# Kernel optimization log

Hardware: AMD Instinct MI355X
Metric: run time of the kernel (lower is better)

Reference implementation:

```python
import jax, jax.numpy as jnp
import numpy as np

HEADS = 4
DIM_HEAD = 128
HIDDEN = HEADS * DIM_HEAD  # 512
DIM = 256
EMBED = 256


def mish(x):
    return x * jnp.tanh(jax.nn.softplus(x))


def setup_inputs() -> dict:
    key = jax.random.key(0)
    k = jax.random.split(key, 7)
    b, a, f, t = 64, 8, DIM, 256
    x = jax.random.normal(k[0], (b, a, f, t), dtype=jnp.float32)
    time = jax.random.normal(k[1], (b, a, EMBED), dtype=jnp.float32)
    # to_qkv: Conv2d(dim, 3*hidden, 1, bias=False) -> weight [3*hidden, dim]
    w_qkv = jax.random.normal(k[2], (3 * HIDDEN, DIM), dtype=jnp.float32) * (1.0 / np.sqrt(DIM))
    # time_mlp: Mish -> Linear(embed, 3*hidden)
    w_time = jax.random.normal(k[3], (3 * HIDDEN, EMBED), dtype=jnp.float32) * (1.0 / np.sqrt(EMBED))
    b_time = jax.random.normal(k[4], (3 * HIDDEN,), dtype=jnp.float32) * 0.01
    # to_out: Conv2d(hidden, dim, 1) with bias
    w_out = jax.random.normal(k[5], (DIM, HIDDEN), dtype=jnp.float32) * (1.0 / np.sqrt(HIDDEN))
    b_out = jax.random.normal(k[6], (DIM,), dtype=jnp.float32) * 0.01
    return {"x": x, "time": time, "w_qkv": w_qkv, "w_time": w_time,
            "b_time": b_time, "w_out": w_out, "b_out": b_out}


def reference(x, time, w_qkv, w_time, b_time, w_out, b_out):
    b, a, f, t = x.shape
    heads, c = HEADS, DIM_HEAD
    # x: b a f t -> b f a t (channels-first for 1x1 conv)
    xp = jnp.transpose(x, (0, 2, 1, 3))  # [b, f, a, t]
    # 1x1 conv == channel GEMM
    qkv = jnp.einsum('of,bfat->boat', w_qkv, xp)  # [b, 3*hidden, a, t]
    # time MLP: Mish -> Linear; bias broadcast over t
    temb = mish(time) @ w_time.T + b_time          # [b, a, 3*hidden]
    temb = jnp.transpose(temb, (0, 2, 1))[..., None]  # [b, 3*hidden, a, 1]
    qkv = qkv + temb
    # 'b (qkv heads c) h w -> qkv (b h) heads c w' with h=a, w=t
    qkv = qkv.reshape(b, 3, heads, c, a, t)
    qkv = jnp.transpose(qkv, (1, 0, 4, 2, 3, 5)).reshape(3, b * a, heads, c, t)
    q, k, v = qkv[0], qkv[1], qkv[2]  # each [(b a), heads, c, t]
    k = jax.nn.softmax(k, axis=-1)
    # linear attention: context over keys/values, then apply to q
    context = jnp.einsum('bhdn,bhen->bhde', k, v)   # [(b a), heads, c, c]
    out = jnp.einsum('bhde,bhdn->bhen', context, q)  # [(b a), heads, c, t]
    # '(b h) heads c w -> b (heads c) h w'
    out = out.reshape(b, a, heads * c, t)
    out = jnp.transpose(out, (0, 2, 1, 3))  # [b, hidden, a, t]
    out = jnp.einsum('of,bfat->boat', w_out, out) + b_out[None, :, None, None]
    # b f a t -> b a f t
    return jnp.transpose(out, (0, 2, 1, 3))
```

## Files before the change

### kernel.cpp

```cpp
#include <hip/hip_runtime.h>

typedef __bf16 bf16;
typedef __bf16 bf16x4 __attribute__((ext_vector_type(4)));
typedef __bf16 bf16x8 __attribute__((ext_vector_type(8)));
typedef float  f32x4  __attribute__((ext_vector_type(4)));

#define TT    256
#define FF    256
#define NS    512

#define TSTR3 36
#define TSZ3  (128 * TSTR3)

#define SCHED0 __builtin_amdgcn_sched_barrier(0)
#define BAR    __builtin_amdgcn_s_barrier()
#define WAITVM(N) asm volatile("s_waitcnt vmcnt(" #N ")" ::: "memory")
#define WAITLGKM0 asm volatile("s_waitcnt lgkmcnt(0)" ::: "memory")
#define SP1 __builtin_amdgcn_s_setprio(1)
#define SP0 __builtin_amdgcn_s_setprio(0)

static __device__ inline f32x4 mfma16(bf16x8 a, bf16x8 b, f32x4 c) {
    return __builtin_amdgcn_mfma_f32_16x16x32_bf16(a, b, c, 0, 0, 0);
}

typedef const __attribute__((address_space(1))) unsigned int* gp_t;
typedef __attribute__((address_space(3))) unsigned int* lp_t;
static __device__ inline void gll16(const bf16* g, bf16* l) {
    __builtin_amdgcn_global_load_lds((gp_t)g, (lp_t)l, 16, 0, 0);
}


static __device__ inline void stage128g(const bf16* __restrict__ g, int ld, bf16* __restrict__ l) {
    int lane = threadIdx.x & 63, wv = threadIdx.x >> 6;
    int r = lane >> 2;
    int c8 = ((lane & 3) ^ ((lane >> 3) & 3)) * 8;
#pragma unroll
    for (int i = 0; i < 2; i++) {
        int row0 = wv * 32 + i * 16;
        gll16(g + (size_t)(row0 + r) * ld + c8, l + row0 * 32);
    }
}
static __device__ inline void stage8(const bf16* __restrict__ g, int ld, bf16* __restrict__ l) {
    int lane = threadIdx.x & 63, wv = threadIdx.x >> 6;
    int r = lane >> 2;
    int c8 = ((lane & 3) ^ ((lane >> 3) & 3)) * 8;
    int row0 = wv * 16;
    gll16(g + (size_t)(row0 + r) * ld + c8, l + row0 * 32);
}
static __device__ inline bf16x8 fragld(const bf16* __restrict__ l, int row0) {
    int lane = threadIdx.x & 63;
    int r15 = lane & 15;
    int kg = (lane >> 4) ^ ((r15 >> 1) & 3);
    return *(const bf16x8*)(l + (row0 + r15) * 32 + kg * 8);
}
static __device__ inline bf16x8 fragld_s(const bf16* __restrict__ l, int row0, int stride) {
    int lane = threadIdx.x & 63;
    return *(const bf16x8*)(l + (row0 + (lane & 15)) * stride + (lane >> 4) * 8);
}

__global__ __launch_bounds__(256) void k_cvt(const float4* __restrict__ src, bf16* __restrict__ dst) {
    int i = blockIdx.x * 256 + threadIdx.x;
    float4 v = src[i];
    bf16x4 o;
    o[0] = (__bf16)v.x; o[1] = (__bf16)v.y; o[2] = (__bf16)v.z; o[3] = (__bf16)v.w;
    *(bf16x4*)(dst + (size_t)i * 4) = o;
}

__global__ __launch_bounds__(256) void k_mish(const float4* __restrict__ src, bf16* __restrict__ dst) {
    int i = blockIdx.x * 256 + threadIdx.x;
    float4 v = src[i];
    float in[4] = {v.x, v.y, v.z, v.w};
    bf16x4 o;
#pragma unroll
    for (int j = 0; j < 4; j++) {
        float sp = log1pf(__expf(in[j]));
        o[j] = (__bf16)(in[j] * tanhf(sp));
    }
    *(bf16x4*)(dst + (size_t)i * 4) = o;
}

__global__ __launch_bounds__(256) void k_xpose(const float* __restrict__ x, bf16* __restrict__ xT) {
    __shared__ float tile[64][65];
    int bid = blockIdx.x;
    int s  = bid >> 4;
    int f0 = ((bid >> 2) & 3) * 64;
    int t0 = (bid & 3) * 64;
    int tid = threadIdx.x;
    int rr = tid >> 4;
    int cc = (tid & 15) * 4;
    const float* xp = x + ((size_t)(s * FF + f0)) * TT + t0;
#pragma unroll
    for (int i = 0; i < 4; i++) {
        int r = i * 16 + rr;
        float4 v = *(const float4*)(xp + (size_t)r * TT + cc);
        tile[r][cc] = v.x; tile[r][cc + 1] = v.y; tile[r][cc + 2] = v.z; tile[r][cc + 3] = v.w;
    }
    __syncthreads();
    bf16* op = xT + ((size_t)(s * TT + t0)) * FF + f0;
#pragma unroll
    for (int i = 0; i < 4; i++) {
        int tr = i * 16 + rr;
        bf16x4 o;
        o[0] = (__bf16)tile[cc][tr];     o[1] = (__bf16)tile[cc + 1][tr];
        o[2] = (__bf16)tile[cc + 2][tr]; o[3] = (__bf16)tile[cc + 3][tr];
        *(bf16x4*)(op + (size_t)tr * FF + cc) = o;
    }
}

__global__ __launch_bounds__(256) void k_temb(const bf16* __restrict__ wt, const bf16* __restrict__ mish,
                                              const float* __restrict__ bt, float* __restrict__ tembT) {
    __shared__ bf16 lA[128 * 32];
    __shared__ bf16 lB[128 * 32];
    int o0 = blockIdx.x * 128, s0 = blockIdx.y * 128;
    int tid = threadIdx.x, wv = tid >> 6, lane = tid & 63, qd = lane >> 4, c = lane & 15;
    f32x4 acc[2][8] = {};
    for (int k0 = 0; k0 < 256; k0 += 32) {
        __syncthreads();
        stage128g(wt + (size_t)o0 * 256 + k0, 256, lA);
        stage128g(mish + (size_t)s0 * 256 + k0, 256, lB);
        __syncthreads();
        bf16x8 a0 = fragld(lA, wv * 32), a1 = fragld(lA, wv * 32 + 16);
#pragma unroll
        for (int nt = 0; nt < 8; nt++) {
            bf16x8 b = fragld(lB, nt * 16);
            acc[0][nt] = mfma16(a0, b, acc[0][nt]);
            acc[1][nt] = mfma16(a1, b, acc[1][nt]);
        }
    }
#pragma unroll
    for (int mt = 0; mt < 2; mt++)
#pragma unroll
        for (int nt = 0; nt < 8; nt++)
#pragma unroll
            for (int r = 0; r < 4; r++) {
                int o = o0 + wv * 32 + mt * 16 + qd * 4 + r;
                int s = s0 + nt * 16 + c;
                tembT[(size_t)o * 512 + s] = acc[mt][nt][r] + bt[o];
            }
}

#define LXF(i)   ((bf16*)(smem + (size_t)(i) * 8192))
#define LWAF(i)  ((bf16*)(smem + 24576 + (size_t)(i) * 8192))
#define LWBF(i)  ((bf16*)(smem + 49152 + (size_t)(i) * 8192))
#define LXF2(i)  ((bf16*)(smem + (size_t)(i) * 8192))
#define LWAF2(i) ((bf16*)(smem + 16384 + (size_t)(i) * 8192))
#define KV_STAGE(st) { int _b = (st) % 3; stage8(xh + (st) * 32, 256, LXF(_b)); \
                       stage8(Wk + (st) * 32, 256, LWAF(_b)); stage8(Wv + (st) * 32, 256, LWBF(_b)); }
#define Q_STAGE2(st) { int _b = (st) & 1; stage8(xh2 + (st) * 32, 256, LXF2(_b)); \
                       stage8(Wq + (st) * 32, 256, LWAF2(_b)); }
__global__ __launch_bounds__(512, 2) void k_fused(const bf16* __restrict__ wqkv, const bf16* __restrict__ xT,
                                                  const float* __restrict__ tembT, bf16* __restrict__ midT) {
    __shared__ __align__(16) char smem[76800];
    bf16*  lk  = (bf16*)(smem);
    bf16*  lv  = (bf16*)(smem + 36864);
    bf16*  lct = (bf16*)(smem + 40960);
    bf16*  lq  = (bf16*)(smem);
    float* ls  = (float*)(smem + 76288);

    int b = blockIdx.x;
    int w = (b & 7) * (4 * NS / 8) + (b >> 3);
    int s = w >> 2, h = w & 3;
    int tid = threadIdx.x, wv = tid >> 6, lane = tid & 63, qd = lane >> 4, c = lane & 15;
    int wa = wv >> 1;
    int wb = wv & 1;
    const bf16* xs = xT + (size_t)s * (TT * FF);
    const bf16* Wq = wqkv + (size_t)(h * 128) * 256;
    const bf16* Wk = wqkv + (size_t)(512 + h * 128) * 256;
    const bf16* Wv = wqkv + (size_t)(1024 + h * 128) * 256;

    if (tid < 128) ls[tid] = 0.f;

    f32x4 cacc[2][4] = {};

    float tbk2[4], tbv2[4];
#pragma unroll
    for (int nt = 0; nt < 4; nt++) {
        int ch = wb * 64 + nt * 16 + c;
        tbk2[nt] = tembT[(size_t)(512 + h * 128 + ch) * 512 + s];
        tbv2[nt] = tembT[(size_t)(1024 + h * 128 + ch) * 512 + s];
    }

    for (int th = 0; th < 2; th++) {
        f32x4 kacc[2][4] = {}, vacc[2][4] = {};
        const bf16* xh = xs + (size_t)th * 128 * 256;
        KV_STAGE(0); SCHED0; KV_STAGE(1); SCHED0; KV_STAGE(2); SCHED0;
#pragma unroll
        for (int p = 0; p < 4; p++) {
            if (p == 3) { WAITVM(0); } else { WAITVM(3); }
            SCHED0; BAR; SCHED0;
            SP1;
#pragma unroll
            for (int u = 0; u < 2; u++) {
                int tb = (2 * p + u) % 3;
                bf16x8 a0 = fragld(LXF(tb), wa * 32);
                bf16x8 a1 = fragld(LXF(tb), wa * 32 + 16);
#pragma unroll
                for (int nt = 0; nt < 4; nt++) {
                    int row = wb * 64 + nt * 16;
                    bf16x8 bk = fragld(LWAF(tb), row);
                    bf16x8 bv = fragld(LWBF(tb), row);
                    kacc[0][nt] = mfma16(a0, bk, kacc[0][nt]);
                    kacc[1][nt] = mfma16(a1, bk, kacc[1][nt]);
                    vacc[0][nt] = mfma16(a0, bv, vacc[0][nt]);
                    vacc[1][nt] = mfma16(a1, bv, vacc[1][nt]);
                }
            }
            SP0;
            SCHED0; BAR; SCHED0;
            if (p == 0) { KV_STAGE(3); KV_STAGE(4); }
            else if (p == 1) { KV_STAGE(5); KV_STAGE(6); }
            else if (p == 2) { KV_STAGE(7); }
            SCHED0;
        }
        {
#pragma unroll
            for (int nt = 0; nt < 4; nt++) {
                int ch = wb * 64 + nt * 16 + c;
                float ps = 0.f;
                bf16x4 ok0, ok1, ov0, ov1;
#pragma unroll
                for (int r = 0; r < 4; r++) {
                    bf16 e0 = (__bf16)__expf(kacc[0][nt][r] + tbk2[nt]);
                    bf16 e1 = (__bf16)__expf(kacc[1][nt][r] + tbk2[nt]);
                    ok0[r] = e0; ok1[r] = e1; ps += (float)e0 + (float)e1;
                    ov0[r] = (__bf16)(vacc[0][nt][r] + tbv2[nt]);
                    ov1[r] = (__bf16)(vacc[1][nt][r] + tbv2[nt]);
                }
                int ad = wa * TSZ3 + ch * TSTR3 + qd * 4;
                *(bf16x4*)(lk + ad)      = ok0;
                *(bf16x4*)(lk + ad + 16) = ok1;
                *(bf16x4*)(lv + ad)      = ov0;
                *(bf16x4*)(lv + ad + 16) = ov1;
                ps += __shfl_xor(ps, 16);
                ps += __shfl_xor(ps, 32);
                if (qd == 0) atomicAdd(&ls[ch], ps);
            }
        }
        __syncthreads();
        SP1;
#pragma unroll
        for (int tc = 0; tc < 4; tc++) {
            bf16x8 a0 = fragld_s(lv + tc * TSZ3, wa * 32, TSTR3);
            bf16x8 a1 = fragld_s(lv + tc * TSZ3, wa * 32 + 16, TSTR3);
#pragma unroll
            for (int nt = 0; nt < 4; nt++) {
                bf16x8 kf = fragld_s(lk + tc * TSZ3, wb * 64 + nt * 16, TSTR3);
                cacc[0][nt] = mfma16(a0, kf, cacc[0][nt]);
                cacc[1][nt] = mfma16(a1, kf, cacc[1][nt]);
            }
        }
        SP0;
        __syncthreads();
    }

    {
        const bf16* xh2 = xs;
        Q_STAGE2(0); SCHED0; Q_STAGE2(1); SCHED0;
    }

#pragma unroll
    for (int ai = 0; ai < 2; ai++)
#pragma unroll
        for (int nt = 0; nt < 4; nt++) {
            int d = wb * 64 + nt * 16 + c;
            float rv = 1.0f / ls[d];
#pragma unroll
            for (int r = 0; r < 4; r++)
                lct[(wa * 32 + ai * 16 + qd * 4 + r) * 136 + d] = (__bf16)(cacc[ai][nt][r] * rv);
        }
    WAITLGKM0;
    SCHED0; BAR; SCHED0;

    float tbq2[2][4];
#pragma unroll
    for (int ai = 0; ai < 2; ai++)
#pragma unroll
        for (int r = 0; r < 4; r++)
            tbq2[ai][r] = tembT[(size_t)(h * 128 + wa * 32 + ai * 16 + qd * 4 + r) * 512 + s];
    for (int th = 0; th < 2; th++) {
        f32x4 qacc[2][4] = {};
        const bf16* xh2 = xs + (size_t)th * 128 * 256;
        if (th == 1) { Q_STAGE2(0); SCHED0; Q_STAGE2(1); SCHED0; }
#pragma unroll
        for (int t = 0; t < 8; t++) {
            if (t == 7) { WAITVM(0); } else { WAITVM(2); }
            SCHED0; BAR; SCHED0;
            SP1;
            {
                bf16x8 a0 = fragld(LWAF2(t & 1), wa * 32);
                bf16x8 a1 = fragld(LWAF2(t & 1), wa * 32 + 16);
#pragma unroll
                for (int nt = 0; nt < 4; nt++) {
                    bf16x8 xf = fragld(LXF2(t & 1), wb * 64 + nt * 16);
                    qacc[0][nt] = mfma16(a0, xf, qacc[0][nt]);
                    qacc[1][nt] = mfma16(a1, xf, qacc[1][nt]);
                }
            }
            SP0;
            SCHED0; BAR; SCHED0;
            if (t + 2 < 8) { Q_STAGE2(t + 2); }
            SCHED0;
        }
        {
#pragma unroll
            for (int nt = 0; nt < 4; nt++) {
                int t = wb * 64 + nt * 16 + c;
#pragma unroll
                for (int ai = 0; ai < 2; ai++) {
                    bf16x4 oq;
#pragma unroll
                    for (int r = 0; r < 4; r++) oq[r] = (__bf16)(qacc[ai][nt][r] + tbq2[ai][r]);
                    *(bf16x4*)(lq + wa * TSZ3 + t * TSTR3 + ai * 16 + qd * 4) = oq;
                }
            }
        }
        __syncthreads();
        f32x4 oacc[2][4] = {};
        SP1;
#pragma unroll
        for (int dd = 0; dd < 4; dd++) {
            bf16x8 a0 = fragld_s(lct + dd * 32, wa * 32, 136);
            bf16x8 a1 = fragld_s(lct + dd * 32, wa * 32 + 16, 136);
#pragma unroll
            for (int nt = 0; nt < 4; nt++) {
                bf16x8 qf = fragld_s(lq + dd * TSZ3, wb * 64 + nt * 16, TSTR3);
                oacc[0][nt] = mfma16(a0, qf, oacc[0][nt]);
                oacc[1][nt] = mfma16(a1, qf, oacc[1][nt]);
            }
        }
        SP0;
#pragma unroll
        for (int nt = 0; nt < 4; nt++)
#pragma unroll
            for (int ai = 0; ai < 2; ai++) {
                int t = th * 128 + wb * 64 + nt * 16 + c;
                int e = wa * 32 + ai * 16 + qd * 4;
                bf16x4 o;
#pragma unroll
                for (int r = 0; r < 4; r++) o[r] = (__bf16)oacc[ai][nt][r];
                *(bf16x4*)(midT + ((size_t)s * 256 + t) * 512 + h * 128 + e) = o;
            }
        __syncthreads();
    }
}

__global__ __launch_bounds__(256) void k_out(const bf16* __restrict__ wo, const bf16* __restrict__ midT,
                                             const float* __restrict__ bo, float* __restrict__ y) {
    __shared__ bf16 lA[3][128 * 32];
    __shared__ bf16 lB[3][128 * 32];
    int b = blockIdx.x;
    int w = (b & 7) * (4 * NS / 8) + (b >> 3);
    int s = w >> 2, j = w & 3;
    int o0 = (j >> 1) * 128, t0 = (j & 1) * 128;
    int tid = threadIdx.x, wv = tid >> 6, lane = tid & 63, qd = lane >> 4, c = lane & 15;
    const bf16* wA = wo + (size_t)o0 * 512;
    const bf16* ms = midT + (size_t)s * 131072 + (size_t)t0 * 512;
    f32x4 acc[2][8] = {};
    stage128g(wA, 512, lA[0]);       stage128g(ms, 512, lB[0]);       SCHED0;
    stage128g(wA + 32, 512, lA[1]);  stage128g(ms + 32, 512, lB[1]);  SCHED0;
    stage128g(wA + 64, 512, lA[2]);  stage128g(ms + 64, 512, lB[2]);  SCHED0;
#pragma unroll
    for (int p = 0; p < 8; p++) {
        if (p == 7) { WAITVM(0); } else { WAITVM(4); }
        SCHED0; BAR; SCHED0;
        SP1;
#pragma unroll
        for (int u = 0; u < 2; u++) {
            int tb = (2 * p + u) % 3;
            bf16x8 a0 = fragld(lA[tb], wv * 32), a1 = fragld(lA[tb], wv * 32 + 16);
#pragma unroll
            for (int nt = 0; nt < 8; nt++) {
                bf16x8 bfr = fragld(lB[tb], nt * 16);
                acc[0][nt] = mfma16(a0, bfr, acc[0][nt]);
                acc[1][nt] = mfma16(a1, bfr, acc[1][nt]);
            }
        }
        SP0;
        SCHED0; BAR; SCHED0;
        {
            int s1 = 2 * p + 3;
            if (s1 < 16)     { stage128g(wA + s1 * 32, 512, lA[s1 % 3]);
                               stage128g(ms + s1 * 32, 512, lB[s1 % 3]); }
            if (s1 + 1 < 16) { stage128g(wA + (s1 + 1) * 32, 512, lA[(s1 + 1) % 3]);
                               stage128g(ms + (s1 + 1) * 32, 512, lB[(s1 + 1) % 3]); }
        }
        SCHED0;
    }
    float bb[2][4];
#pragma unroll
    for (int mt = 0; mt < 2; mt++)
#pragma unroll
        for (int r = 0; r < 4; r++)
            bb[mt][r] = bo[o0 + wv * 32 + mt * 16 + qd * 4 + r];
#pragma unroll
    for (int mt = 0; mt < 2; mt++)
#pragma unroll
        for (int nt = 0; nt < 8; nt++)
#pragma unroll
            for (int r = 0; r < 4; r++) {
                int o = o0 + wv * 32 + mt * 16 + qd * 4 + r;
                int t = t0 + nt * 16 + c;
                y[((size_t)(s * 256 + o)) * 256 + t] = acc[mt][nt][r] + bb[mt][r];
            }
}

extern "C" void kernel_launch(void* const* d_in, const int* in_sizes, int n_in,
                              void* d_out, int out_size, void* d_ws, size_t ws_size,
                              hipStream_t stream) {
    const float* x      = (const float*)d_in[0];
    const float* time_  = (const float*)d_in[1];
    const float* w_qkv  = (const float*)d_in[2];
    const float* w_time = (const float*)d_in[3];
    const float* b_time = (const float*)d_in[4];
    const float* w_out  = (const float*)d_in[5];
    const float* b_out  = (const float*)d_in[6];
    float* y = (float*)d_out;
    char* ws = (char*)d_ws;

    bf16*  wqkv_bf  = (bf16*)(ws + 0);
    bf16*  wtime_bf = (bf16*)(ws + 786432);
    bf16*  wout_bf  = (bf16*)(ws + 1572864);
    bf16*  mish_bf  = (bf16*)(ws + 1835008);
    float* tembT    = (float*)(ws + 2097152);
    bf16*  xT       = (bf16*)(ws + 5242880);
    bf16*  midT     = (bf16*)(ws + 72351744);

    k_cvt<<<384, 256, 0, stream>>>((const float4*)w_qkv, wqkv_bf);
    k_cvt<<<384, 256, 0, stream>>>((const float4*)w_time, wtime_bf);
    k_cvt<<<128, 256, 0, stream>>>((const float4*)w_out, wout_bf);
    k_mish<<<128, 256, 0, stream>>>((const float4*)time_, mish_bf);
    k_temb<<<dim3(12, 4), 256, 0, stream>>>(wtime_bf, mish_bf, b_time, tembT);

    k_xpose<<<NS * 16, 256, 0, stream>>>(x, xT);
    k_fused<<<NS * 4, 512, 0, stream>>>(wqkv_bf, xT, tembT, midT);
    k_out<<<4 * NS, 256, 0, stream>>>(wout_bf, midT, b_out, y);
}
```

Baseline: 650.6 us.

## Fuse Q projection into K/V staging loop to reuse staged x tiles

Result: no change. 640.9 us (-1.5%).

```diff
diff --git a/kernel.cpp b/kernel.cpp
--- a/kernel.cpp
+++ b/kernel.cpp
@@ -142,20 +142,18 @@
 #define LXF(i)   ((bf16*)(smem + (size_t)(i) * 8192))
 #define LWAF(i)  ((bf16*)(smem + 24576 + (size_t)(i) * 8192))
 #define LWBF(i)  ((bf16*)(smem + 49152 + (size_t)(i) * 8192))
-#define LXF2(i)  ((bf16*)(smem + (size_t)(i) * 8192))
-#define LWAF2(i) ((bf16*)(smem + 16384 + (size_t)(i) * 8192))
-#define KV_STAGE(st) { int _b = (st) % 3; stage8(xh + (st) * 32, 256, LXF(_b)); \
-                       stage8(Wk + (st) * 32, 256, LWAF(_b)); stage8(Wv + (st) * 32, 256, LWBF(_b)); }
-#define Q_STAGE2(st) { int _b = (st) & 1; stage8(xh2 + (st) * 32, 256, LXF2(_b)); \
-                       stage8(Wq + (st) * 32, 256, LWAF2(_b)); }
+#define LWQF(i)  ((bf16*)(smem + 73728 + (size_t)(i) * 8192))
+#define KVQ_STAGE(st) { int _b = (st) % 3; stage8(xh + (st) * 32, 256, LXF(_b)); \
+                        stage8(Wk + (st) * 32, 256, LWAF(_b)); stage8(Wv + (st) * 32, 256, LWBF(_b)); \
+                        stage8(Wq + (st) * 32, 256, LWQF(_b)); }
 __global__ __launch_bounds__(512, 2) void k_fused(const bf16* __restrict__ wqkv, const bf16* __restrict__ xT,
                                                   const float* __restrict__ tembT, bf16* __restrict__ midT) {
-    __shared__ __align__(16) char smem[76800];
+    __shared__ __align__(16) char smem[111104];
     bf16*  lk  = (bf16*)(smem);
     bf16*  lv  = (bf16*)(smem + 36864);
-    bf16*  lct = (bf16*)(smem + 40960);
-    bf16*  lq  = (bf16*)(smem);
-    float* ls  = (float*)(smem + 76288);
+    bf16*  lct = (bf16*)(smem);
+    bf16*  lq  = (bf16*)(smem + 36864);
+    float* ls  = (float*)(smem + 110592);
 
     int b = blockIdx.x;
     int w = (b & 7) * (4 * NS / 8) + (b >> 3);
@@ -171,6 +169,7 @@
     if (tid < 128) ls[tid] = 0.f;
 
     f32x4 cacc[2][4] = {};
+    f32x4 qacc[2][2][4] = {};
 
     float tbk2[4], tbv2[4];
 #pragma unroll
@@ -180,13 +179,14 @@
         tbv2[nt] = tembT[(size_t)(1024 + h * 128 + ch) * 512 + s];
     }
 
+#pragma unroll
     for (int th = 0; th < 2; th++) {
         f32x4 kacc[2][4] = {}, vacc[2][4] = {};
         const bf16* xh = xs + (size_t)th * 128 * 256;
-        KV_STAGE(0); SCHED0; KV_STAGE(1); SCHED0; KV_STAGE(2); SCHED0;
+        KVQ_STAGE(0); SCHED0; KVQ_STAGE(1); SCHED0; KVQ_STAGE(2); SCHED0;
 #pragma unroll
         for (int p = 0; p < 4; p++) {
-            if (p == 3) { WAITVM(0); } else { WAITVM(3); }
+            if (p == 3) { WAITVM(0); } else { WAITVM(4); }
             SCHED0; BAR; SCHED0;
             SP1;
 #pragma unroll
@@ -194,22 +194,27 @@
                 int tb = (2 * p + u) % 3;
                 bf16x8 a0 = fragld(LXF(tb), wa * 32);
                 bf16x8 a1 = fragld(LXF(tb), wa * 32 + 16);
+                bf16x8 qa0 = fragld(LWQF(tb), wa * 32);
+                bf16x8 qa1 = fragld(LWQF(tb), wa * 32 + 16);
 #pragma unroll
                 for (int nt = 0; nt < 4; nt++) {
                     int row = wb * 64 + nt * 16;
                     bf16x8 bk = fragld(LWAF(tb), row);
                     bf16x8 bv = fragld(LWBF(tb), row);
+                    bf16x8 xb = fragld(LXF(tb), row);
                     kacc[0][nt] = mfma16(a0, bk, kacc[0][nt]);
                     kacc[1][nt] = mfma16(a1, bk, kacc[1][nt]);
                     vacc[0][nt] = mfma16(a0, bv, vacc[0][nt]);
                     vacc[1][nt] = mfma16(a1, bv, vacc[1][nt]);
+                    qacc[th][0][nt] = mfma16(qa0, xb, qacc[th][0][nt]);
+                    qacc[th][1][nt] = mfma16(qa1, xb, qacc[th][1][nt]);
                 }
             }
             SP0;
             SCHED0; BAR; SCHED0;
-            if (p == 0) { KV_STAGE(3); KV_STAGE(4); }
-            else if (p == 1) { KV_STAGE(5); KV_STAGE(6); }
-            else if (p == 2) { KV_STAGE(7); }
+            if (p == 0) { KVQ_STAGE(3); KVQ_STAGE(4); }
+            else if (p == 1) { KVQ_STAGE(5); KVQ_STAGE(6); }
+            else if (p == 2) { KVQ_STAGE(7); }
             SCHED0;
         }
         {
@@ -253,10 +258,12 @@
         __syncthreads();
     }
 
-    {
-        const bf16* xh2 = xs;
-        Q_STAGE2(0); SCHED0; Q_STAGE2(1); SCHED0;
-    }
+    float tbq[2][4];
+#pragma unroll
+    for (int ai = 0; ai < 2; ai++)
+#pragma unroll
+        for (int r = 0; r < 4; r++)
+            tbq[ai][r] = tembT[(size_t)(h * 128 + wa * 32 + ai * 16 + qd * 4 + r) * 512 + s];
 
 #pragma unroll
     for (int ai = 0; ai < 2; ai++)
@@ -268,53 +275,26 @@
             for (int r = 0; r < 4; r++)
                 lct[(wa * 32 + ai * 16 + qd * 4 + r) * 136 + d] = (__bf16)(cacc[ai][nt][r] * rv);
         }
-    WAITLGKM0;
-    SCHED0; BAR; SCHED0;
-
-    float tbq2[2][4];
-#pragma unroll
-    for (int ai = 0; ai < 2; ai++)
-#pragma unroll
-        for (int r = 0; r < 4; r++)
-            tbq2[ai][r] = tembT[(size_t)(h * 128 + wa * 32 + ai * 16 + qd * 4 + r) * 512 + s];
+#pragma unroll
     for (int th = 0; th < 2; th++) {
-        f32x4 qacc[2][4] = {};
-        const bf16* xh2 = xs + (size_t)th * 128 * 256;
-        if (th == 1) { Q_STAGE2(0); SCHED0; Q_STAGE2(1); SCHED0; }
-#pragma unroll
-        for (int t = 0; t < 8; t++) {
-            if (t == 7) { WAITVM(0); } else { WAITVM(2); }
-            SCHED0; BAR; SCHED0;
-            SP1;
-            {
-                bf16x8 a0 = fragld(LWAF2(t & 1), wa * 32);
-                bf16x8 a1 = fragld(LWAF2(t & 1), wa * 32 + 16);
-#pragma unroll
-                for (int nt = 0; nt < 4; nt++) {
-                    bf16x8 xf = fragld(LXF2(t & 1), wb * 64 + nt * 16);
-                    qacc[0][nt] = mfma16(a0, xf, qacc[0][nt]);
-                    qacc[1][nt] = mfma16(a1, xf, qacc[1][nt]);
-                }
-            }
-            SP0;
-            SCHED0; BAR; SCHED0;
-            if (t + 2 < 8) { Q_STAGE2(t + 2); }
-            SCHED0;
-        }
-        {
-#pragma unroll
-            for (int nt = 0; nt < 4; nt++) {
-                int t = wb * 64 + nt * 16 + c;
-#pragma unroll
-                for (int ai = 0; ai < 2; ai++) {
-                    bf16x4 oq;
-#pragma unroll
-                    for (int r = 0; r < 4; r++) oq[r] = (__bf16)(qacc[ai][nt][r] + tbq2[ai][r]);
-                    *(bf16x4*)(lq + wa * TSZ3 + t * TSTR3 + ai * 16 + qd * 4) = oq;
-                }
-            }
-        }
-        __syncthreads();
+        bf16* lqh = lq + (size_t)th * 4 * TSZ3;
+#pragma unroll
+        for (int nt = 0; nt < 4; nt++) {
+            int t = wb * 64 + nt * 16 + c;
+#pragma unroll
+            for (int ai = 0; ai < 2; ai++) {
+                bf16x4 oq;
+#pragma unroll
+                for (int r = 0; r < 4; r++) oq[r] = (__bf16)(qacc[th][ai][nt][r] + tbq[ai][r]);
+                *(bf16x4*)(lqh + wa * TSZ3 + t * TSTR3 + ai * 16 + qd * 4) = oq;
+            }
+        }
+    }
+    __syncthreads();
+
+#pragma unroll
+    for (int th = 0; th < 2; th++) {
+        const bf16* lqh = lq + (size_t)th * 4 * TSZ3;
         f32x4 oacc[2][4] = {};
         SP1;
 #pragma unroll
@@ -323,7 +303,7 @@
             bf16x8 a1 = fragld_s(lct + dd * 32, wa * 32 + 16, 136);
 #pragma unroll
             for (int nt = 0; nt < 4; nt++) {
-                bf16x8 qf = fragld_s(lq + dd * TSZ3, wb * 64 + nt * 16, TSTR3);
+                bf16x8 qf = fragld_s(lqh + dd * TSZ3, wb * 64 + nt * 16, TSTR3);
                 oacc[0][nt] = mfma16(a0, qf, oacc[0][nt]);
                 oacc[1][nt] = mfma16(a1, qf, oacc[1][nt]);
             }
@@ -340,7 +320,6 @@
                 for (int r = 0; r < 4; r++) o[r] = (__bf16)oacc[ai][nt][r];
                 *(bf16x4*)(midT + ((size_t)s * 256 + t) * 512 + h * 128 + e) = o;
             }
-        __syncthreads();
     }
 }
 
```
